# Performance work log

Hardware: AMD Instinct MI355X
Metric: run time of the kernel (lower is better)

## Reference

```python
import jax, jax.numpy as jnp
import numpy as np

B = 16384      # batch size
D = 512        # state_dim (= number of graph nodes)
HID = 512      # hidden_dim of main GCN blocks
EH = 32        # hidden dim of ENSO GCN blocks
K = 2          # fourier_modes
OMEGA = 2.0 * np.pi / 12.0


def setup_inputs() -> dict:
    ks = jax.random.split(jax.random.key(0), 20)
    def w(k, shape, scale=0.05):
        return (jax.random.normal(k, shape) * scale).astype(jnp.float32)
    inp = {
        "x": jax.random.normal(ks[0], (B, D), dtype=jnp.float32),
        "t": jax.random.uniform(ks[1], (1,), dtype=jnp.float32) * 12.0,
        "fourier_coeffs": w(ks[2], (D, D, 2 * K + 1), 0.1),
        # quadratic_graph: GCN(D->HID) -> ReLU -> GCN(HID->D)
        "quad_W1": w(ks[3], (D, HID)), "quad_b1": jnp.zeros((HID,), jnp.float32),
        "quad_W2": w(ks[4], (HID, D)), "quad_b2": jnp.zeros((D,), jnp.float32),
        # cubic_graph
        "cubic_W1": w(ks[5], (D, HID)), "cubic_b1": jnp.zeros((HID,), jnp.float32),
        "cubic_W2": w(ks[6], (HID, D)), "cubic_b2": jnp.zeros((D,), jnp.float32),
        # enso_T_graph: GCN(5->32) -> ReLU -> GCN(32->1)
        "ensoT_W1": w(ks[7], (5, EH)), "ensoT_b1": jnp.zeros((EH,), jnp.float32),
        "ensoT_W2": w(ks[8], (EH, 1)), "ensoT_b2": jnp.zeros((1,), jnp.float32),
        # enso_H_graph
        "ensoH_W1": w(ks[9], (5, EH)), "ensoH_b1": jnp.zeros((EH,), jnp.float32),
        "ensoH_W2": w(ks[10], (EH, 1)), "ensoH_b2": jnp.zeros((1,), jnp.float32),
    }
    return inp


def _gcn2(feat, W1, b1, W2, b2):
    # Fully-connected graph + self-loops => normalized adjacency P = (1/N) 11^T.
    # All node rows are identical (x expanded over nodes), so P @ X == X and every
    # node's output is identical: the 2-layer GCN collapses to two dense GEMMs.
    h = jax.nn.relu(feat @ W1 + b1)
    return h @ W2 + b2


def reference(x, t, fourier_coeffs,
              quad_W1, quad_b1, quad_W2, quad_b2,
              cubic_W1, cubic_b1, cubic_W2, cubic_b2,
              ensoT_W1, ensoT_b1, ensoT_W2, ensoT_b2,
              ensoH_W1, ensoH_b1, ensoH_W2, ensoH_b2):
    ts = t[0]
    # --- Seasonal linear operator L(t) = C0 + sum_k Ck^c cos(k w t) + Ck^s sin(k w t)
    L = fourier_coeffs[:, :, 0]
    for k in range(1, K + 1):
        L = L + fourier_coeffs[:, :, 2 * k - 1] * jnp.cos(k * OMEGA * ts)
        L = L + fourier_coeffs[:, :, 2 * k] * jnp.sin(k * OMEGA * ts)
    linear_term = jnp.einsum('ij,bj->bi', L, x)  # [B, D]

    # --- Graph nonlinear terms (per-node outputs identical; mean over feature dim)
    quad = _gcn2(x, quad_W1, quad_b1, quad_W2, quad_b2)        # [B, D]
    cubic = _gcn2(x, cubic_W1, cubic_b1, cubic_W2, cubic_b2)   # [B, D]
    # torch: out[node] identical for all nodes; .mean(dim=1) over features -> same
    # scalar replicated across the state dimension.
    quad_terms = jnp.broadcast_to(quad.mean(axis=1, keepdims=True), (x.shape[0], D))
    cubic_terms = jnp.broadcast_to(cubic.mean(axis=1, keepdims=True), (x.shape[0], D))
    nonlinear = quad_terms + cubic_terms

    # --- ENSO-specific physics (state_dim >= 2)
    T = x[:, 0:1]
    H = x[:, 1:2]
    fT = jnp.concatenate([T, H, T * T, T * H, T * T * T], axis=1)   # [B, 5]
    fH = jnp.concatenate([T, H, T * T, T * H, T * H * H], axis=1)   # [B, 5]
    cT = _gcn2(fT, ensoT_W1, ensoT_b1, ensoT_W2, ensoT_b2)  # [B, 1]
    cH = _gcn2(fH, ensoH_W1, ensoH_b1, ensoH_W2, ensoH_b2)  # [B, 1]
    pad = jnp.zeros((x.shape[0], D - 2), dtype=x.dtype)
    nonlinear = nonlinear + jnp.concatenate([cT, cH, pad], axis=1)

    return linear_term + nonlinear
```

## Files before the change

### kernel.cpp

```cpp
#include <hip/hip_runtime.h>


#define OMEGA_F 0.5235987755982988f

typedef __attribute__((ext_vector_type(8))) short short8;
typedef __attribute__((ext_vector_type(4))) float f32x4;

__device__ __forceinline__ unsigned short f2bf(float f) {
  union { float f; unsigned int u; } a;
  a.f = f;
  unsigned int u = a.u;
  return (unsigned short)((u + 0x7fffu + ((u >> 16) & 1u)) >> 16);
}

__device__ __forceinline__ void gload16(const void* g, void* l) {
  __builtin_amdgcn_global_load_lds(
      (const __attribute__((address_space(1))) unsigned int*)g,
      (__attribute__((address_space(3))) unsigned int*)l, 16, 0, 0);
}

__global__ void prep_conv(const float* __restrict__ fc, const float* __restrict__ qW1,
                          const float* __restrict__ cW1, const float* __restrict__ t,
                          const float* __restrict__ qW2, const float* __restrict__ cW2,
                          const float* __restrict__ qb2, const float* __restrict__ cb2,
                          const float4* __restrict__ x4, const float* __restrict__ x,
                          const float* __restrict__ tW1, const float* __restrict__ tb1,
                          const float* __restrict__ tW2, const float* __restrict__ tb2,
                          const float* __restrict__ hW1, const float* __restrict__ hb1,
                          const float* __restrict__ hW2, const float* __restrict__ hb2,
                          unsigned short* __restrict__ WT, uint2* __restrict__ xb,
                          float* __restrict__ qw2m, float* __restrict__ cw2m,
                          float* __restrict__ b2m, float* __restrict__ cT,
                          float* __restrict__ cH, float* __restrict__ rowadd) {
  int b = blockIdx.x, tdx = threadIdx.x;
  if (b < 3072) {
    int idx = b * 256 + tdx;
    int n = idx >> 9;
    int k = idx & 511;
    float v;
    if (n < 512) {
      float th = OMEGA_F * t[0];
      float s1, c1, s2, c2;
      sincosf(th, &s1, &c1);
      sincosf(2.0f * th, &s2, &c2);
      const float* p = fc + ((size_t)n * 512 + k) * 5;
      v = p[0] + p[1] * c1 + p[2] * s1 + p[3] * c2 + p[4] * s2;
    } else if (n < 1024) {
      v = qW1[(size_t)k * 512 + (n - 512)];
    } else {
      v = cW1[(size_t)k * 512 + (n - 1024)];
    }
    WT[idx] = f2bf(v);
  } else if (b < 3076) {
    int bb = b - 3072;
    const float* W = (bb < 2) ? qW2 : cW2;
    float* o = (bb < 2) ? qw2m : cw2m;
    int h = (bb & 1) * 256 + tdx;
    const float4* row = (const float4*)(W + (size_t)h * 512);
    float s = 0.f;
    for (int i = 0; i < 128; ++i) { float4 v = row[i]; s += (v.x + v.y) + (v.z + v.w); }
    o[h] = s * (1.0f / 512.0f);
  } else if (b == 3076) {
    __shared__ float sm[256];
    sm[tdx] = qb2[tdx] + qb2[tdx + 256];
    __syncthreads();
    for (int w = 128; w > 0; w >>= 1) { if (tdx < w) sm[tdx] += sm[tdx + w]; __syncthreads(); }
    if (tdx == 0) b2m[0] = sm[0] * (1.0f / 512.0f);
    __syncthreads();
    sm[tdx] = cb2[tdx] + cb2[tdx + 256];
    __syncthreads();
    for (int w = 128; w > 0; w >>= 1) { if (tdx < w) sm[tdx] += sm[tdx + w]; __syncthreads(); }
    if (tdx == 0) b2m[1] = sm[0] * (1.0f / 512.0f);
  } else if (b < 3077 + 8192) {
    int i = (b - 3077) * 256 + tdx;
    float4 v = x4[i];
    uint2 r;
    r.x = (unsigned)f2bf(v.x) | ((unsigned)f2bf(v.y) << 16);
    r.y = (unsigned)f2bf(v.z) | ((unsigned)f2bf(v.w) << 16);
    xb[i] = r;
  } else {
    int row = (b - 11269) * 256 + tdx;
    rowadd[row] = 0.f;
    float T = x[(size_t)row * 512];
    float H = x[(size_t)row * 512 + 1];
    float fT[5] = {T, H, T * T, T * H, T * T * T};
    float fH[5] = {T, H, T * T, T * H, T * H * H};
    float sT = tb2[0], sH = hb2[0];
#pragma unroll 4
    for (int e = 0; e < 32; ++e) {
      float a1 = tb1[e], a2 = hb1[e];
#pragma unroll
      for (int f = 0; f < 5; ++f) {
        a1 += fT[f] * tW1[f * 32 + e];
        a2 += fH[f] * hW1[f * 32 + e];
      }
      sT += fmaxf(a1, 0.f) * tW2[e];
      sH += fmaxf(a2, 0.f) * hW2[e];
    }
    cT[row] = sT;
    cH[row] = sH;
  }
}

#define GEMM_MAINLOOP(A_, Bt_, MB_, NB_)                                          \
  const int tid = threadIdx.x;                                                    \
  const int lane = tid & 63;                                                      \
  const int wave = tid >> 6;                                                      \
  const int wm = wave & 1;                                                        \
  const int wn = wave >> 1;                                                       \
  const int m_base = (MB_);                                                       \
  const int n_base = (NB_);                                                       \
  const int lrow = lane & 15;                                                     \
  const int l7 = lrow & 7;                                                        \
  const int kgrp = lane >> 4;                                                     \
  const int srow = lane >> 3;                                                     \
  const int sk = ((lane & 7) ^ srow) * 8;                                         \
  const unsigned short* gA0 = (A_) + (size_t)(m_base + wave * 8 + srow) * 512 + sk; \
  const unsigned short* gA1 = gA0 + 32 * 512;                                     \
  const unsigned short* gA2 = gA0 + 64 * 512;                                     \
  const unsigned short* gA3 = gA0 + 96 * 512;                                     \
  const unsigned short* gB0 = (Bt_) + (size_t)(n_base + wave * 8 + srow) * 512 + sk;\
  const unsigned short* gB1 = gB0 + 32 * 512;                                     \
  const unsigned short* gB2 = gB0 + 64 * 512;                                     \
  const unsigned short* gB3 = gB0 + 96 * 512;                                     \
  unsigned short* lA0 = As + wave * 512;                                          \
  unsigned short* lA1 = As + (4 + wave) * 512;                                    \
  unsigned short* lA2 = As + (8 + wave) * 512;                                    \
  unsigned short* lA3 = As + (12 + wave) * 512;                                   \
  unsigned short* lB0 = Bs + wave * 512;                                          \
  unsigned short* lB1 = Bs + (4 + wave) * 512;                                    \
  unsigned short* lB2 = Bs + (8 + wave) * 512;                                    \
  unsigned short* lB3 = Bs + (12 + wave) * 512;                                   \
  f32x4 acc[4][4];                                                                \
  _Pragma("unroll") for (int i = 0; i < 4; ++i)                                   \
      _Pragma("unroll") for (int j = 0; j < 4; ++j)                               \
          acc[i][j] = (f32x4){0.f, 0.f, 0.f, 0.f};                                \
  for (int k0 = 0; k0 < 512; k0 += 64) {                                          \
    gload16(gA0, lA0); gload16(gA1, lA1); gload16(gA2, lA2); gload16(gA3, lA3);   \
    gload16(gB0, lB0); gload16(gB1, lB1); gload16(gB2, lB2); gload16(gB3, lB3);   \
    gA0 += 64; gA1 += 64; gA2 += 64; gA3 += 64;                                   \
    gB0 += 64; gB1 += 64; gB2 += 64; gB3 += 64;                                   \
    __syncthreads();                                                              \
    _Pragma("unroll") for (int h = 0; h < 2; ++h) {                               \
      short8 af[4], bfr[4];                                                       \
      const int ks = ((h * 4 + kgrp) ^ l7) * 8;                                   \
      _Pragma("unroll") for (int i = 0; i < 4; ++i)                               \
          af[i] = *(const short8*)(&As[(wm * 64 + i * 16 + lrow) * 64 + ks]);     \
      _Pragma("unroll") for (int j = 0; j < 4; ++j)                               \
          bfr[j] = *(const short8*)(&Bs[(wn * 64 + j * 16 + lrow) * 64 + ks]);    \
      _Pragma("unroll") for (int i = 0; i < 4; ++i)                               \
          _Pragma("unroll") for (int j = 0; j < 4; ++j)                           \
              acc[i][j] = __builtin_amdgcn_mfma_f32_16x16x32_bf16(af[i], bfr[j],  \
                                                                  acc[i][j], 0, 0, 0); \
    }                                                                             \
    __syncthreads();                                                              \
  }

__global__ __launch_bounds__(256) void nl_gemm(
    const unsigned short* __restrict__ A,
    const unsigned short* __restrict__ Bt,
    const float* __restrict__ qb1, const float* __restrict__ cb1,
    const float* __restrict__ qw2m, const float* __restrict__ cw2m,
    float* __restrict__ rowadd) {
  __shared__ unsigned short As[128 * 64];
  __shared__ unsigned short Bs[128 * 64];
  float rs[4][4];
#pragma unroll
  for (int i = 0; i < 4; ++i)
#pragma unroll
    for (int r = 0; r < 4; ++r) rs[i][r] = 0.f;

  for (int t = 0; t < 2; ++t) {
    GEMM_MAINLOOP(A, Bt, blockIdx.x * 128, (blockIdx.y * 2 + t) * 128)
    const bool isq = (n_base < 512);
    const float* b1 = isq ? qb1 : cb1;
    const float* w2m = isq ? qw2m : cw2m;
    const int cb0 = (isq ? n_base : n_base - 512) + wn * 64 + lrow;
#pragma unroll
    for (int j = 0; j < 4; ++j) {
      int col = cb0 + j * 16;
      float bb = b1[col];
      float ww = w2m[col];
#pragma unroll
      for (int i = 0; i < 4; ++i)
#pragma unroll
        for (int r = 0; r < 4; ++r)
          rs[i][r] += fmaxf(acc[i][j][r] + bb, 0.f) * ww;
    }
  }

  const int lane_e = threadIdx.x & 63;
  const int wm_e = (threadIdx.x >> 6) & 1;
  const int rbase = blockIdx.x * 128 + wm_e * 64 + (lane_e >> 4) * 4;
#pragma unroll
  for (int i = 0; i < 4; ++i)
#pragma unroll
    for (int r = 0; r < 4; ++r) {
      float v = rs[i][r];
      v += __shfl_xor(v, 1, 64);
      v += __shfl_xor(v, 2, 64);
      v += __shfl_xor(v, 4, 64);
      v += __shfl_xor(v, 8, 64);
      if ((lane_e & 15) == 0) atomicAdd(&rowadd[rbase + i * 16 + r], v);
    }
}

__global__ __launch_bounds__(256) void lin_gemm(
    const unsigned short* __restrict__ A,
    const unsigned short* __restrict__ Bt,
    const float* __restrict__ rowadd, const float* __restrict__ b2m,
    const float* __restrict__ cT, const float* __restrict__ cH,
    float* __restrict__ out) {
  __shared__ unsigned short As[128 * 64];
  __shared__ unsigned short Bs[128 * 64];
  GEMM_MAINLOOP(A, Bt, blockIdx.x * 128, blockIdx.y * 128)
  const int rbase = m_base + wm * 64 + (lane >> 4) * 4;
  const float b2s = b2m[0] + b2m[1];
  float ra[4][4];
#pragma unroll
  for (int i = 0; i < 4; ++i)
#pragma unroll
    for (int r = 0; r < 4; ++r) ra[i][r] = rowadd[rbase + i * 16 + r] + b2s;
#pragma unroll
  for (int j = 0; j < 4; ++j) {
    int col = n_base + wn * 64 + j * 16 + lrow;
#pragma unroll
    for (int i = 0; i < 4; ++i)
#pragma unroll
      for (int r = 0; r < 4; ++r) {
        int row = rbase + i * 16 + r;
        float v = acc[i][j][r] + ra[i][r];
        if (col == 0) v += cT[row];
        if (col == 1) v += cH[row];
        out[(size_t)row * 512 + col] = v;
      }
  }
}

extern "C" void kernel_launch(void* const* d_in, const int* in_sizes, int n_in,
                              void* d_out, int out_size, void* d_ws, size_t ws_size,
                              hipStream_t stream) {
  const float* x   = (const float*)d_in[0];
  const float* t   = (const float*)d_in[1];
  const float* fc  = (const float*)d_in[2];
  const float* qW1 = (const float*)d_in[3];
  const float* qb1 = (const float*)d_in[4];
  const float* qW2 = (const float*)d_in[5];
  const float* qb2 = (const float*)d_in[6];
  const float* cW1 = (const float*)d_in[7];
  const float* cb1 = (const float*)d_in[8];
  const float* cW2 = (const float*)d_in[9];
  const float* cb2 = (const float*)d_in[10];
  const float* tW1 = (const float*)d_in[11];
  const float* tb1 = (const float*)d_in[12];
  const float* tW2 = (const float*)d_in[13];
  const float* tb2 = (const float*)d_in[14];
  const float* hW1 = (const float*)d_in[15];
  const float* hb1 = (const float*)d_in[16];
  const float* hW2 = (const float*)d_in[17];
  const float* hb2 = (const float*)d_in[18];
  float* out = (float*)d_out;

  char* ws = (char*)d_ws;
  unsigned short* WT = (unsigned short*)(ws);
  unsigned short* xb = (unsigned short*)(ws + 1572864);
  float* qw2m   = (float*)(ws + 18350080);
  float* cw2m   = (float*)(ws + 18352128);
  float* b2m    = (float*)(ws + 18354176);
  float* cT     = (float*)(ws + 18354432);
  float* cH     = (float*)(ws + 18419968);
  float* rowadd = (float*)(ws + 18485504);

  prep_conv<<<11333, 256, 0, stream>>>(fc, qW1, cW1, t, qW2, cW2, qb2, cb2,
                                       (const float4*)x, x,
                                       tW1, tb1, tW2, tb2, hW1, hb1, hW2, hb2,
                                       WT, (uint2*)xb, qw2m, cw2m, b2m, cT, cH,
                                       rowadd);
  nl_gemm<<<dim3(128, 4), 256, 0, stream>>>(xb, WT + (size_t)512 * 512,
                                            qb1, cb1, qw2m, cw2m, rowadd);
  lin_gemm<<<dim3(128, 4), 256, 0, stream>>>(xb, WT, rowadd, b2m, cT, cH, out);
}
```

Baseline: 171.7 us.

## Widen GEMM tiles to 128x256 so each A tile feeds two B tiles

The GEMM main loop now computes a 128x256 output tile per block: it loads one A tile and two B tiles per k-step and keeps two accumulator sets. In nl_gemm this replaces the loop over two 128-wide column tiles, so the A tile is read once instead of twice. lin_gemm's grid is halved in y, so each block covers 256 columns. The aim is fewer A reloads and better MFMA-to-load ratio, at the cost of 32 more accumulator registers per thread, more LDS (48KB), and fewer blocks in lin_gemm (256 blocks), which may reduce occupancy.

```diff
diff --git a/kernel.cpp b/kernel.cpp
--- a/kernel.cpp
+++ b/kernel.cpp
@@ -102,14 +102,14 @@
   }
 }
 
-#define GEMM_MAINLOOP(A_, Bt_, MB_, NB_)                                          \
+#define WIDE_MAINLOOP(A_, Bt_, MB_, N0_)                                          \
   const int tid = threadIdx.x;                                                    \
   const int lane = tid & 63;                                                      \
   const int wave = tid >> 6;                                                      \
   const int wm = wave & 1;                                                        \
   const int wn = wave >> 1;                                                       \
   const int m_base = (MB_);                                                       \
-  const int n_base = (NB_);                                                       \
+  const int n0 = (N0_);                                                           \
   const int lrow = lane & 15;                                                     \
   const int l7 = lrow & 7;                                                        \
   const int kgrp = lane >> 4;                                                     \
@@ -119,79 +119,95 @@
   const unsigned short* gA1 = gA0 + 32 * 512;                                     \
   const unsigned short* gA2 = gA0 + 64 * 512;                                     \
   const unsigned short* gA3 = gA0 + 96 * 512;                                     \
-  const unsigned short* gB0 = (Bt_) + (size_t)(n_base + wave * 8 + srow) * 512 + sk;\
-  const unsigned short* gB1 = gB0 + 32 * 512;                                     \
-  const unsigned short* gB2 = gB0 + 64 * 512;                                     \
-  const unsigned short* gB3 = gB0 + 96 * 512;                                     \
+  const unsigned short* gB00 = (Bt_) + (size_t)(n0 + wave * 8 + srow) * 512 + sk; \
+  const unsigned short* gB01 = gB00 + 32 * 512;                                   \
+  const unsigned short* gB02 = gB00 + 64 * 512;                                   \
+  const unsigned short* gB03 = gB00 + 96 * 512;                                   \
+  const unsigned short* gB10 = gB00 + 128 * 512;                                  \
+  const unsigned short* gB11 = gB00 + 160 * 512;                                  \
+  const unsigned short* gB12 = gB00 + 192 * 512;                                  \
+  const unsigned short* gB13 = gB00 + 224 * 512;                                  \
   unsigned short* lA0 = As + wave * 512;                                          \
   unsigned short* lA1 = As + (4 + wave) * 512;                                    \
   unsigned short* lA2 = As + (8 + wave) * 512;                                    \
   unsigned short* lA3 = As + (12 + wave) * 512;                                   \
-  unsigned short* lB0 = Bs + wave * 512;                                          \
-  unsigned short* lB1 = Bs + (4 + wave) * 512;                                    \
-  unsigned short* lB2 = Bs + (8 + wave) * 512;                                    \
-  unsigned short* lB3 = Bs + (12 + wave) * 512;                                   \
-  f32x4 acc[4][4];                                                                \
+  unsigned short* lB00 = B0s + wave * 512;                                        \
+  unsigned short* lB01 = B0s + (4 + wave) * 512;                                  \
+  unsigned short* lB02 = B0s + (8 + wave) * 512;                                  \
+  unsigned short* lB03 = B0s + (12 + wave) * 512;                                 \
+  unsigned short* lB10 = B1s + wave * 512;                                        \
+  unsigned short* lB11 = B1s + (4 + wave) * 512;                                  \
+  unsigned short* lB12 = B1s + (8 + wave) * 512;                                  \
+  unsigned short* lB13 = B1s + (12 + wave) * 512;                                 \
+  f32x4 acc0[4][4], acc1[4][4];                                                   \
   _Pragma("unroll") for (int i = 0; i < 4; ++i)                                   \
-      _Pragma("unroll") for (int j = 0; j < 4; ++j)                               \
-          acc[i][j] = (f32x4){0.f, 0.f, 0.f, 0.f};                                \
+      _Pragma("unroll") for (int j = 0; j < 4; ++j) {                             \
+        acc0[i][j] = (f32x4){0.f, 0.f, 0.f, 0.f};                                 \
+        acc1[i][j] = (f32x4){0.f, 0.f, 0.f, 0.f};                                 \
+      }                                                                           \
   for (int k0 = 0; k0 < 512; k0 += 64) {                                          \
     gload16(gA0, lA0); gload16(gA1, lA1); gload16(gA2, lA2); gload16(gA3, lA3);   \
-    gload16(gB0, lB0); gload16(gB1, lB1); gload16(gB2, lB2); gload16(gB3, lB3);   \
+    gload16(gB00, lB00); gload16(gB01, lB01); gload16(gB02, lB02); gload16(gB03, lB03); \
+    gload16(gB10, lB10); gload16(gB11, lB11); gload16(gB12, lB12); gload16(gB13, lB13); \
     gA0 += 64; gA1 += 64; gA2 += 64; gA3 += 64;                                   \
-    gB0 += 64; gB1 += 64; gB2 += 64; gB3 += 64;                                   \
+    gB00 += 64; gB01 += 64; gB02 += 64; gB03 += 64;                               \
+    gB10 += 64; gB11 += 64; gB12 += 64; gB13 += 64;                               \
     __syncthreads();                                                              \
     _Pragma("unroll") for (int h = 0; h < 2; ++h) {                               \
-      short8 af[4], bfr[4];                                                       \
+      short8 af[4], b0f[4], b1f[4];                                               \
       const int ks = ((h * 4 + kgrp) ^ l7) * 8;                                   \
       _Pragma("unroll") for (int i = 0; i < 4; ++i)                               \
           af[i] = *(const short8*)(&As[(wm * 64 + i * 16 + lrow) * 64 + ks]);     \
-      _Pragma("unroll") for (int j = 0; j < 4; ++j)                               \
-          bfr[j] = *(const short8*)(&Bs[(wn * 64 + j * 16 + lrow) * 64 + ks]);    \
+      _Pragma("unroll") for (int j = 0; j < 4; ++j) {                             \
+        b0f[j] = *(const short8*)(&B0s[(wn * 64 + j * 16 + lrow) * 64 + ks]);     \
+        b1f[j] = *(const short8*)(&B1s[(wn * 64 + j * 16 + lrow) * 64 + ks]);     \
+      }                                                                           \
       _Pragma("unroll") for (int i = 0; i < 4; ++i)                               \
-          _Pragma("unroll") for (int j = 0; j < 4; ++j)                           \
-              acc[i][j] = __builtin_amdgcn_mfma_f32_16x16x32_bf16(af[i], bfr[j],  \
-                                                                  acc[i][j], 0, 0, 0); \
+          _Pragma("unroll") for (int j = 0; j < 4; ++j) {                         \
+            acc0[i][j] = __builtin_amdgcn_mfma_f32_16x16x32_bf16(af[i], b0f[j],   \
+                                                                 acc0[i][j], 0, 0, 0); \
+            acc1[i][j] = __builtin_amdgcn_mfma_f32_16x16x32_bf16(af[i], b1f[j],   \
+                                                                 acc1[i][j], 0, 0, 0); \
+          }                                                                       \
     }                                                                             \
     __syncthreads();                                                              \
   }
 
-__global__ __launch_bounds__(256) void nl_gemm(
+__global__ __launch_bounds__(256, 2) void nl_gemm(
     const unsigned short* __restrict__ A,
     const unsigned short* __restrict__ Bt,
     const float* __restrict__ qb1, const float* __restrict__ cb1,
     const float* __restrict__ qw2m, const float* __restrict__ cw2m,
     float* __restrict__ rowadd) {
   __shared__ unsigned short As[128 * 64];
-  __shared__ unsigned short Bs[128 * 64];
+  __shared__ unsigned short B0s[128 * 64];
+  __shared__ unsigned short B1s[128 * 64];
+  WIDE_MAINLOOP(A, Bt, blockIdx.x * 128, blockIdx.y * 256)
+
+  const bool isq = (n0 < 512);
+  const float* b1p = isq ? qb1 : cb1;
+  const float* w2m = isq ? qw2m : cw2m;
+  const int cb0 = (isq ? n0 : n0 - 512) + wn * 64 + lrow;
   float rs[4][4];
 #pragma unroll
   for (int i = 0; i < 4; ++i)
 #pragma unroll
     for (int r = 0; r < 4; ++r) rs[i][r] = 0.f;
-
-  for (int t = 0; t < 2; ++t) {
-    GEMM_MAINLOOP(A, Bt, blockIdx.x * 128, (blockIdx.y * 2 + t) * 128)
-    const bool isq = (n_base < 512);
-    const float* b1 = isq ? qb1 : cb1;
-    const float* w2m = isq ? qw2m : cw2m;
-    const int cb0 = (isq ? n_base : n_base - 512) + wn * 64 + lrow;
-#pragma unroll
-    for (int j = 0; j < 4; ++j) {
-      int col = cb0 + j * 16;
-      float bb = b1[col];
-      float ww = w2m[col];
-#pragma unroll
-      for (int i = 0; i < 4; ++i)
-#pragma unroll
-        for (int r = 0; r < 4; ++r)
-          rs[i][r] += fmaxf(acc[i][j][r] + bb, 0.f) * ww;
-    }
+#pragma unroll
+  for (int j = 0; j < 4; ++j) {
+    int col0 = cb0 + j * 16;
+    float bb0 = b1p[col0], ww0 = w2m[col0];
+    float bb1 = b1p[col0 + 128], ww1 = w2m[col0 + 128];
+#pragma unroll
+    for (int i = 0; i < 4; ++i)
+#pragma unroll
+      for (int r = 0; r < 4; ++r) {
+        rs[i][r] += fmaxf(acc0[i][j][r] + bb0, 0.f) * ww0;
+        rs[i][r] += fmaxf(acc1[i][j][r] + bb1, 0.f) * ww1;
+      }
   }
 
-  const int lane_e = threadIdx.x & 63;
-  const int wm_e = (threadIdx.x >> 6) & 1;
-  const int rbase = blockIdx.x * 128 + wm_e * 64 + (lane_e >> 4) * 4;
+  const int rbase = m_base + wm * 64 + kgrp * 4;
 #pragma unroll
   for (int i = 0; i < 4; ++i)
 #pragma unroll
@@ -201,20 +217,22 @@
       v += __shfl_xor(v, 2, 64);
       v += __shfl_xor(v, 4, 64);
       v += __shfl_xor(v, 8, 64);
-      if ((lane_e & 15) == 0) atomicAdd(&rowadd[rbase + i * 16 + r], v);
+      if (lrow == 0) atomicAdd(&rowadd[rbase + i * 16 + r], v);
     }
 }
 
-__global__ __launch_bounds__(256) void lin_gemm(
+__global__ __launch_bounds__(256, 2) void lin_gemm(
     const unsigned short* __restrict__ A,
     const unsigned short* __restrict__ Bt,
     const float* __restrict__ rowadd, const float* __restrict__ b2m,
     const float* __restrict__ cT, const float* __restrict__ cH,
     float* __restrict__ out) {
   __shared__ unsigned short As[128 * 64];
-  __shared__ unsigned short Bs[128 * 64];
-  GEMM_MAINLOOP(A, Bt, blockIdx.x * 128, blockIdx.y * 128)
-  const int rbase = m_base + wm * 64 + (lane >> 4) * 4;
+  __shared__ unsigned short B0s[128 * 64];
+  __shared__ unsigned short B1s[128 * 64];
+  WIDE_MAINLOOP(A, Bt, blockIdx.x * 128, blockIdx.y * 256)
+
+  const int rbase = m_base + wm * 64 + kgrp * 4;
   const float b2s = b2m[0] + b2m[1];
   float ra[4][4];
 #pragma unroll
@@ -223,16 +241,19 @@
     for (int r = 0; r < 4; ++r) ra[i][r] = rowadd[rbase + i * 16 + r] + b2s;
 #pragma unroll
   for (int j = 0; j < 4; ++j) {
-    int col = n_base + wn * 64 + j * 16 + lrow;
+    const int col0 = n0 + wn * 64 + j * 16 + lrow;
+    const int col1 = col0 + 128;
 #pragma unroll
     for (int i = 0; i < 4; ++i)
 #pragma unroll
       for (int r = 0; r < 4; ++r) {
-        int row = rbase + i * 16 + r;
-        float v = acc[i][j][r] + ra[i][r];
-        if (col == 0) v += cT[row];
-        if (col == 1) v += cH[row];
-        out[(size_t)row * 512 + col] = v;
+        const int row = rbase + i * 16 + r;
+        float v0 = acc0[i][j][r] + ra[i][r];
+        float v1 = acc1[i][j][r] + ra[i][r];
+        if (col0 == 0) v0 += cT[row];
+        if (col0 == 1) v0 += cH[row];
+        out[(size_t)row * 512 + col0] = v0;
+        out[(size_t)row * 512 + col1] = v1;
       }
   }
 }
@@ -278,5 +299,5 @@
                                        rowadd);
   nl_gemm<<<dim3(128, 4), 256, 0, stream>>>(xb, WT + (size_t)512 * 512,
                                             qb1, cb1, qw2m, cw2m, rowadd);
-  lin_gemm<<<dim3(128, 4), 256, 0, stream>>>(xb, WT, rowadd, b2m, cT, cH, out);
-}
+  lin_gemm<<<dim3(128, 2), 256, 0, stream>>>(xb, WT, rowadd, b2m, cT, cH, out);
+}
```

After: 176.6 us. +2.9%, slower.
